# Kernel optimization log

Measured on AMD Instinct MI355X. Metric: run time of the kernel, lower is better.

The kernel has to match this reference:

```python
import jax, jax.numpy as jnp
import numpy as np
import math

D_MODEL = 1024
LAYER_ID = 6
NUM_LAYERS = 12
B = 8
T = 2048


def setup_inputs() -> dict:
    key = jax.random.key(0)
    ks = jax.random.split(key, 5)
    r01 = LAYER_ID / (NUM_LAYERS - 1)
    r1a0 = 1.0 - LAYER_ID / NUM_LAYERS
    h = np.arange(D_MODEL, dtype=np.float32)
    w = (-5.0 + 8.0 * (h / (D_MODEL - 1)) ** (0.7 + 1.3 * r01)).astype(np.float32)
    zigzag = np.array([(i + 1) % 3 - 1 for i in range(D_MODEL)], np.float32) * 0.5
    u = (np.ones(D_MODEL, np.float32) * math.log(0.3) + zigzag).astype(np.float32)
    xinit = (h / D_MODEL).astype(np.float32)
    tmk = (xinit ** r1a0).reshape(1, 1, D_MODEL).astype(np.float32)
    tmv = (tmk + 0.3 * r01).astype(np.float32)
    tmr = (xinit ** (0.5 * r1a0)).reshape(1, 1, D_MODEL).astype(np.float32)
    s = 1.0 / math.sqrt(D_MODEL)
    Wk = jax.random.normal(ks[0], (D_MODEL, D_MODEL), jnp.float32) * s
    Wv = jax.random.normal(ks[1], (D_MODEL, D_MODEL), jnp.float32) * s
    Wr = jax.random.normal(ks[2], (D_MODEL, D_MODEL), jnp.float32) * s
    Wo = jax.random.normal(ks[3], (D_MODEL, D_MODEL), jnp.float32) * s
    x = jax.random.normal(ks[4], (B, T, D_MODEL), jnp.float32)
    return dict(
        x=x,
        w=jnp.asarray(w), u=jnp.asarray(u),
        time_mix_k=jnp.asarray(tmk), time_mix_v=jnpp if False else jnp.asarray(tmv), time_mix_r=jnp.asarray(tmr),
        Wk=Wk, Wv=Wv, Wr=Wr, Wo=Wo,
    )


def _wkv(w, u, k, v):
    # w,u: [C] (raw params); k,v: [B,T,C]. Numerically-stable RWKV scan.
    wn = -jnp.exp(w)  # decay (negative)

    def step(carry, kv):
        aa, bb, pp = carry  # each [B,C]
        kt, vt = kv         # [B,C]
        ww = u + kt
        p = jnp.maximum(pp, ww)
        e1 = jnp.exp(pp - p)
        e2 = jnp.exp(ww - p)
        y = (e1 * aa + e2 * vt) / (e1 * bb + e2)
        ww2 = pp + wn
        p2 = jnp.maximum(ww2, kt)
        e1b = jnp.exp(ww2 - p2)
        e2b = jnp.exp(kt - p2)
        return (e1b * aa + e2b * vt, e1b * bb + e2b, p2), y

    Bd, Td, Cd = k.shape
    init = (jnp.zeros((Bd, Cd), k.dtype), jnp.zeros((Bd, Cd), k.dtype),
            jnp.full((Bd, Cd), -1e38, k.dtype))
    kT = jnp.swapaxes(k, 0, 1)  # [T,B,C]
    vT = jnp.swapaxes(v, 0, 1)
    _, ys = jax.lax.scan(step, init, (kT, vT))
    return jnp.swapaxes(ys, 0, 1)  # [B,T,C]


def reference(x, w, u, time_mix_k, time_mix_v, time_mix_r, Wk, Wv, Wr, Wo):
    # token shift: zero-pad one step at the front of time, drop last
    xs = jnp.pad(x, ((0, 0), (1, 0), (0, 0)))[:, :-1]
    xk = x * time_mix_k + xs * (1.0 - time_mix_k)
    xv = x * time_mix_v + xs * (1.0 - time_mix_v)
    xr = x * time_mix_r + xs * (1.0 - time_mix_r)
    k = jnp.einsum('btc,dc->btd', xk, Wk)
    v = jnp.einsum('btc,dc->btd', xv, Wv)
    r = jnp.einsum('btc,dc->btd', xr, Wr)
    wkv = _wkv(w, u, k, v)
    rwkv = jax.nn.sigmoid(r) * wkv
    return jnp.einsum('btc,dc->btd', rwkv, Wo)
```

## Files before the change

### kernel.cpp

```cpp
#include <hip/hip_runtime.h>
#include <hip/hip_bf16.h>
#include <stdint.h>

#define DM     1024
#define BATCH  8
#define SEQ    2048
#define MROWS  (BATCH * SEQ)
#define NCH    16
#define CHL    (SEQ / NCH)
#define CSTR   544

typedef unsigned short u16;
typedef __attribute__((ext_vector_type(8))) __bf16 bf16x8;
typedef __attribute__((ext_vector_type(4))) float  f32x4;

#define MB (1024ull * 1024ull)

__device__ __forceinline__ u16 f2bf(float f) {
    unsigned u = __float_as_uint(f);
    u += 0x7fffu + ((u >> 16) & 1u);
    return (u16)(u >> 16);
}
__device__ __forceinline__ float bf2f(u16 h) {
    return __uint_as_float(((unsigned)h) << 16);
}

__device__ __forceinline__ bool in_f32(const void* wraw) {
    return ((*(const unsigned*)wraw) & 0xFFFFu) == 0u;
}

__device__ __forceinline__ void ld16_lds(const u16* g, u16* l) {
    __builtin_amdgcn_global_load_lds(
        (const __attribute__((address_space(1))) void*)g,
        (__attribute__((address_space(3))) void*)l, 16, 0, 0);
}

__global__ __launch_bounds__(256) void mix_tile(
    const void* __restrict__ xraw,
    const void* __restrict__ tmkraw,
    const void* __restrict__ tmvraw,
    const void* __restrict__ tmrraw,
    const void* __restrict__ wraw,
    u16* __restrict__ xk, u16* __restrict__ xv, u16* __restrict__ xr)
{
    __shared__ u16 xt[18 * 1024];
    const bool f32i = in_f32(wraw);
    const int r0  = blockIdx.x * 16;
    const int t0  = r0 & (SEQ - 1);
    const int tid = threadIdx.x;
    const int c4  = tid * 4;

    float mk[4], mv[4], mr[4];
    if (f32i) {
        #pragma unroll
        for (int j = 0; j < 4; ++j) {
            mk[j] = ((const float*)tmkraw)[c4 + j];
            mv[j] = ((const float*)tmvraw)[c4 + j];
            mr[j] = ((const float*)tmrraw)[c4 + j];
        }
    } else {
        union { u16 h[4]; uint2 u; } a, b, c;
        a.u = *(const uint2*)((const u16*)tmkraw + c4);
        b.u = *(const uint2*)((const u16*)tmvraw + c4);
        c.u = *(const uint2*)((const u16*)tmrraw + c4);
        #pragma unroll
        for (int j = 0; j < 4; ++j) {
            mk[j] = bf2f(a.h[j]); mv[j] = bf2f(b.h[j]); mr[j] = bf2f(c.h[j]);
        }
    }

    #pragma unroll
    for (int p = 0; p < 9; ++p) {
        int lr = 2 * p + (tid >> 7);
        int gr = r0 - 1 + lr;
        if (lr == 0 && t0 == 0) gr = r0;
        if (gr >= MROWS) gr = r0;
        if (f32i) {
            const float* gp = (const float*)xraw + (size_t)gr * DM + (tid & 127) * 8;
            union { u16 h[8]; uint4 u; } t;
            #pragma unroll
            for (int j = 0; j < 8; ++j) t.h[j] = f2bf(gp[j]);
            *(uint4*)&xt[p * 2048 + tid * 8] = t.u;
        } else {
            const u16* gp = (const u16*)xraw + (size_t)gr * DM + (tid & 127) * 8;
            ld16_lds(gp, &xt[p * 2048 + (tid >> 6) * 512]);
        }
    }
    __syncthreads();

    const size_t obase = (size_t)r0 * DM + c4;
    #pragma unroll 4
    for (int rr = 0; rr < 16; ++rr) {
        union { u16 h[4]; uint2 u; } xa, xsv, ok, ov, orr;
        xa.u = *(const uint2*)&xt[(rr + 1) * 1024 + c4];
        float xf[4], sf[4];
        if (rr == 0 && t0 == 0) {
            #pragma unroll
            for (int j = 0; j < 4; ++j) sf[j] = 0.f;
        } else {
            xsv.u = *(const uint2*)&xt[rr * 1024 + c4];
            #pragma unroll
            for (int j = 0; j < 4; ++j) sf[j] = bf2f(xsv.h[j]);
        }
        #pragma unroll
        for (int j = 0; j < 4; ++j) xf[j] = bf2f(xa.h[j]);
        #pragma unroll
        for (int j = 0; j < 4; ++j) {
            float d = xf[j] - sf[j];
            ok.h[j]  = f2bf(sf[j] + mk[j] * d);
            ov.h[j]  = f2bf(sf[j] + mv[j] * d);
            orr.h[j] = f2bf(sf[j] + mr[j] * d);
        }
        size_t o = obase + (size_t)rr * DM;
        *(uint2*)(xk + o) = ok.u;
        *(uint2*)(xv + o) = ov.u;
        *(uint2*)(xr + o) = orr.u;
    }
}

__global__ void cast_w(const void* __restrict__ Wraw,
                       const void* __restrict__ wflag,
                       u16* __restrict__ Wb)
{
    int i = (blockIdx.x * 256 + threadIdx.x) << 2;
    if (in_f32(wflag)) {
        float4 wv = *(const float4*)((const float*)Wraw + i);
        union { u16 h[4]; uint2 u; } p;
        p.h[0] = f2bf(wv.x); p.h[1] = f2bf(wv.y);
        p.h[2] = f2bf(wv.z); p.h[3] = f2bf(wv.w);
        *(uint2*)(Wb + i) = p.u;
    } else {
        *(uint2*)(Wb + i) = *(const uint2*)((const u16*)Wraw + i);
    }
}

template <int NZ>
__global__ __launch_bounds__(256) void gemm_bt(
    const u16* __restrict__ A0, const u16* __restrict__ A1, const u16* __restrict__ A2,
    const u16* __restrict__ B0, const u16* __restrict__ B1, const u16* __restrict__ B2,
    void* __restrict__ C0, void* __restrict__ C1, void* __restrict__ C2,
    int c0f32)
{
    __shared__ u16 As[16 * CSTR];
    __shared__ u16 Bs[16 * CSTR];

    const int lin = blockIdx.x + (blockIdx.y << 3) + (blockIdx.z << 10);
    const int xcd = lin & 7;
    const int idx = lin >> 3;
    const int bxe = idx & 7;
    const int t   = idx >> 3;
    const int bye = xcd + ((t & 15) << 3);
    const int z   = t >> 4;

    const u16* A = (z == 0) ? A0 : (z == 1) ? A1 : A2;
    const u16* B = (z == 0) ? B0 : (z == 1) ? B1 : B2;
    void*      C = (z == 0) ? C0 : (z == 1) ? C1 : C2;
    const bool f32out = (z == 0) && c0f32;

    const int tid  = threadIdx.x;
    const int wave = tid >> 6, lane = tid & 63;
    const int wm   = wave >> 1, wn = wave & 1;
    const int lr   = lane & 15, quad = lane >> 4;
    const int tm   = bye * 128, tn = bxe * 128;
    const int srow  = lane >> 3;
    const int skoff = (lane & 7) * 8;

    f32x4 acc[4][4] = {};

    for (int k0 = 0; k0 < DM; k0 += 64) {
        #pragma unroll
        for (int i2 = 0; i2 < 4; ++i2) {
            int ch  = wave * 4 + i2;
            int row = ch * 8 + srow;
            ld16_lds(A + (size_t)(tm + row) * DM + k0 + skoff, &As[ch * CSTR]);
            ld16_lds(B + (size_t)(tn + row) * DM + k0 + skoff, &Bs[ch * CSTR]);
        }
        __syncthreads();
        #pragma unroll
        for (int kk2 = 0; kk2 < 2; ++kk2) {
            bf16x8 af[4], bfg[4];
            #pragma unroll
            for (int mi = 0; mi < 4; ++mi) {
                int r = wm * 64 + mi * 16 + lr;
                af[mi] = *(const bf16x8*)&As[(r >> 3) * CSTR + (r & 7) * 64 + kk2 * 32 + quad * 8];
            }
            #pragma unroll
            for (int ni = 0; ni < 4; ++ni) {
                int r = wn * 64 + ni * 16 + lr;
                bfg[ni] = *(const bf16x8*)&Bs[(r >> 3) * CSTR + (r & 7) * 64 + kk2 * 32 + quad * 8];
            }
            #pragma unroll
            for (int mi = 0; mi < 4; ++mi)
                #pragma unroll
                for (int ni = 0; ni < 4; ++ni)
                    acc[mi][ni] = __builtin_amdgcn_mfma_f32_16x16x32_bf16(
                        af[mi], bfg[ni], acc[mi][ni], 0, 0, 0);
        }
        __syncthreads();
    }
    #pragma unroll
    for (int mi = 0; mi < 4; ++mi)
        #pragma unroll
        for (int ni = 0; ni < 4; ++ni)
            #pragma unroll
            for (int r = 0; r < 4; ++r) {
                int row = tm + wm * 64 + mi * 16 + quad * 4 + r;
                int col = tn + wn * 64 + ni * 16 + lr;
                float v = acc[mi][ni][r];
                if (f32out) ((float*)C)[(size_t)row * DM + col] = v;
                else        ((u16*)C)[(size_t)row * DM + col]   = f2bf(v);
            }
}

__device__ __forceinline__ float ldval(const float* p) { return *p; }
__device__ __forceinline__ float ldval(const u16*  p) { return bf2f(*p); }

template <typename KT>
__global__ __launch_bounds__(256) void wkv_phase1(
    const KT* __restrict__ kk, const u16* __restrict__ vv,
    const void* __restrict__ wraw,
    float* __restrict__ sa, float* __restrict__ sb, float* __restrict__ sp)
{
    const int gid = blockIdx.x * 256 + threadIdx.x;
    const int c   = gid & (DM - 1);
    const int ch  = (gid >> 10) & (NCH - 1);
    const int b   = gid >> 14;
    float wc = in_f32(wraw) ? ((const float*)wraw)[c] : bf2f(((const u16*)wraw)[c]);
    const float wn = -__expf(wc);

    const size_t base = ((size_t)b * SEQ + (size_t)ch * CHL) * DM + c;
    float la = 0.f, lb = 0.f, lp = -1e38f;

    float kb[8], vb[8];
    #pragma unroll
    for (int j = 0; j < 8; ++j) {
        size_t id = base + (size_t)j * DM;
        kb[j] = ldval(kk + id); vb[j] = ldval(vv + id);
    }
    for (int t0 = 0; t0 < CHL; t0 += 8) {
        const bool more = (t0 + 8) < CHL;
        float kn[8], vn[8];
        if (more) {
            size_t nb = base + (size_t)(t0 + 8) * DM;
            #pragma unroll
            for (int j = 0; j < 8; ++j) {
                size_t id = nb + (size_t)j * DM;
                kn[j] = ldval(kk + id); vn[j] = ldval(vv + id);
            }
        }
        #pragma unroll
        for (int j = 0; j < 8; ++j) {
            const float kt = kb[j], vt = vb[j];
            const float w2 = lp + wn;
            const float p2 = fmaxf(w2, kt);
            const float e1 = __expf(w2 - p2);
            const float e2 = __expf(kt - p2);
            la = e1 * la + e2 * vt;
            lb = e1 * lb + e2;
            lp = p2;
        }
        if (more) {
            #pragma unroll
            for (int j = 0; j < 8; ++j) { kb[j] = kn[j]; vb[j] = vn[j]; }
        }
    }
    const int sidx = ((b * NCH + ch) << 10) + c;
    sa[sidx] = la; sb[sidx] = lb; sp[sidx] = lp;
}

__global__ __launch_bounds__(256) void wkv_combine(
    float* __restrict__ sa, float* __restrict__ sb, float* __restrict__ sp,
    const void* __restrict__ wraw)
{
    const int gid = blockIdx.x * 256 + threadIdx.x;
    const int c   = gid & (DM - 1);
    const int b   = gid >> 10;
    float wc = in_f32(wraw) ? ((const float*)wraw)[c] : bf2f(((const u16*)wraw)[c]);
    const float lamL = -__expf(wc) * (float)CHL;

    float aa = 0.f, bb = 0.f, pp = -1e38f;
    #pragma unroll
    for (int j = 0; j < NCH; ++j) {
        const int idx = ((b * NCH + j) << 10) + c;
        const float la = sa[idx], lb = sb[idx], lp = sp[idx];
        sa[idx] = aa; sb[idx] = bb; sp[idx] = pp;
        const float w2 = pp + lamL;
        const float np = fmaxf(w2, lp);
        const float e1 = __expf(w2 - np);
        const float e2 = __expf(lp - np);
        aa = e1 * aa + e2 * la;
        bb = e1 * bb + e2 * lb;
        pp = np;
    }
}

template <typename KT>
__global__ __launch_bounds__(256) void wkv_phase3(
    const KT* __restrict__ kk, const u16* __restrict__ vv,
    const u16* __restrict__ rr,
    const float* __restrict__ sa, const float* __restrict__ sb,
    const float* __restrict__ sp,
    const void* __restrict__ wraw, const void* __restrict__ uraw,
    u16* __restrict__ out)
{
    const int gid = blockIdx.x * 256 + threadIdx.x;
    const int c   = gid & (DM - 1);
    const int ch  = (gid >> 10) & (NCH - 1);
    const int b   = gid >> 14;
    float wc, uc;
    if (in_f32(wraw)) {
        wc = ((const float*)wraw)[c]; uc = ((const float*)uraw)[c];
    } else {
        wc = bf2f(((const u16*)wraw)[c]); uc = bf2f(((const u16*)uraw)[c]);
    }
    const float wn = -__expf(wc);
    const float uu = uc;

    const int sidx = ((b * NCH + ch) << 10) + c;
    float aa = sa[sidx], bb = sb[sidx], pp = sp[sidx];

    const size_t base = ((size_t)b * SEQ + (size_t)ch * CHL) * DM + c;

    float kb[8], vb[8], rb[8];
    #pragma unroll
    for (int j = 0; j < 8; ++j) {
        size_t id = base + (size_t)j * DM;
        kb[j] = ldval(kk + id); vb[j] = ldval(vv + id); rb[j] = ldval(rr + id);
    }
    for (int t0 = 0; t0 < CHL; t0 += 8) {
        const bool more = (t0 + 8) < CHL;
        float kn[8], vn[8], rn[8];
        if (more) {
            size_t nb = base + (size_t)(t0 + 8) * DM;
            #pragma unroll
            for (int j = 0; j < 8; ++j) {
                size_t id = nb + (size_t)j * DM;
                kn[j] = ldval(kk + id); vn[j] = ldval(vv + id); rn[j] = ldval(rr + id);
            }
        }
        #pragma unroll
        for (int j = 0; j < 8; ++j) {
            const float kt = kb[j], vt = vb[j], rt = rb[j];
            const float ww = uu + kt;
            const float p  = fmaxf(pp, ww);
            const float e1 = __expf(pp - p);
            const float e2 = __expf(ww - p);
            const float y  = (e1 * aa + e2 * vt) / (e1 * bb + e2);
            const float w2 = pp + wn;
            const float p2 = fmaxf(w2, kt);
            const float e1b = __expf(w2 - p2);
            const float e2b = __expf(kt - p2);
            aa = e1b * aa + e2b * vt;
            bb = e1b * bb + e2b;
            pp = p2;
            const float sr = 1.f / (1.f + __expf(-rt));
            out[base + (size_t)(t0 + j) * DM] = f2bf(sr * y);
        }
        if (more) {
            #pragma unroll
            for (int j = 0; j < 8; ++j) { kb[j] = kn[j]; vb[j] = vn[j]; rb[j] = rn[j]; }
        }
    }
}

extern "C" void kernel_launch(void* const* d_in, const int* in_sizes, int n_in,
                              void* d_out, int out_size, void* d_ws, size_t ws_size,
                              hipStream_t stream)
{
    const void* x   = d_in[0];
    const void* w   = d_in[1];
    const void* u   = d_in[2];
    const void* tmk = d_in[3];
    const void* tmv = d_in[4];
    const void* tmr = d_in[5];
    const void* Wk  = d_in[6];
    const void* Wv  = d_in[7];
    const void* Wr  = d_in[8];
    const void* Wo  = d_in[9];

    char* base = (char*)d_ws;
    const bool kf32 = ws_size >= 168 * MB;
    u16* Wkb  = (u16*)(base);
    u16* Wvb  = (u16*)(base + 2 * MB);
    u16* Wrb  = (u16*)(base + 4 * MB);
    u16* Wob  = (u16*)(base + 6 * MB);
    u16* xk   = (u16*)(base + 8 * MB);
    u16* xv   = (u16*)(base + 40 * MB);
    u16* xr   = (u16*)(base + 72 * MB);
    void* kbuf = (void*)(base + 104 * MB);
    u16* vb   = xk;
    u16* rb   = xv;
    u16* rwkv = xr;
    float* sa   = (float*)(base);
    float* sbuf = (float*)(base + 512 * 1024);
    float* sp   = (float*)(base + 1024 * 1024);

    cast_w<<<DM * DM / 1024, 256, 0, stream>>>(Wk, w, Wkb);
    cast_w<<<DM * DM / 1024, 256, 0, stream>>>(Wv, w, Wvb);
    cast_w<<<DM * DM / 1024, 256, 0, stream>>>(Wr, w, Wrb);
    cast_w<<<DM * DM / 1024, 256, 0, stream>>>(Wo, w, Wob);
    mix_tile<<<MROWS / 16, 256, 0, stream>>>(x, tmk, tmv, tmr, w, xk, xv, xr);

    gemm_bt<3><<<dim3(8, 128, 3), 256, 0, stream>>>(
        xk, xv, xr, Wkb, Wvb, Wrb, kbuf, vb, rb, kf32 ? 1 : 0);

    const int scan_threads = BATCH * NCH * DM;
    if (kf32) {
        wkv_phase1<float><<<scan_threads / 256, 256, 0, stream>>>(
            (const float*)kbuf, vb, w, sa, sbuf, sp);
        wkv_combine<<<BATCH * DM / 256, 256, 0, stream>>>(sa, sbuf, sp, w);
        wkv_phase3<float><<<scan_threads / 256, 256, 0, stream>>>(
            (const float*)kbuf, vb, rb, sa, sbuf, sp, w, u, rwkv);
    } else {
        wkv_phase1<u16><<<scan_threads / 256, 256, 0, stream>>>(
            (const u16*)kbuf, vb, w, sa, sbuf, sp);
        wkv_combine<<<BATCH * DM / 256, 256, 0, stream>>>(sa, sbuf, sp, w);
        wkv_phase3<u16><<<scan_threads / 256, 256, 0, stream>>>(
            (const u16*)kbuf, vb, rb, sa, sbuf, sp, w, u, rwkv);
    }

    gemm_bt<1><<<dim3(8, 128, 1), 256, 0, stream>>>(
        rwkv, rwkv, rwkv, Wob, Wob, Wob, d_out, d_out, d_out, 1);
}
```

Measured before the change: 413.9 us.

## Rewrite bf16 GEMM with 256x256 tiles, double-buffered LDS and XOR swizzle

The GEMM kernel moves from 128x128 tiles with 4 waves to 256x256 tiles with 8 waves, so each block reuses more operand data per load. LDS is now double-buffered, with the next tile's A and B loads issued between MFMA groups under explicit waitcnt and barrier control. An XOR swizzle replaces the padded LDS stride to avoid bank conflicts. This uses 128KB of LDS per block and more accumulator registers, which lowers occupancy, and the grid shrinks to 768 and 256 blocks, which risks poorer load balance across CUs.

```diff
diff --git a/kernel.cpp b/kernel.cpp
--- a/kernel.cpp
+++ b/kernel.cpp
@@ -8,7 +8,7 @@
 #define MROWS  (BATCH * SEQ)
 #define NCH    16
 #define CHL    (SEQ / NCH)
-#define CSTR   544
+#define NT     (DM / 64)
 
 typedef unsigned short u16;
 typedef __attribute__((ext_vector_type(8))) __bf16 bf16x8;
@@ -135,78 +135,127 @@
 }
 
 template <int NZ>
-__global__ __launch_bounds__(256) void gemm_bt(
+__global__ __launch_bounds__(512) void gemm_bt(
     const u16* __restrict__ A0, const u16* __restrict__ A1, const u16* __restrict__ A2,
     const u16* __restrict__ B0, const u16* __restrict__ B1, const u16* __restrict__ B2,
     void* __restrict__ C0, void* __restrict__ C1, void* __restrict__ C2,
     int c0f32)
 {
-    __shared__ u16 As[16 * CSTR];
-    __shared__ u16 Bs[16 * CSTR];
-
-    const int lin = blockIdx.x + (blockIdx.y << 3) + (blockIdx.z << 10);
+    __shared__ u16 As[2][256 * 64];
+    __shared__ u16 Bs[2][256 * 64];
+
+    const int lin = blockIdx.x;
     const int xcd = lin & 7;
     const int idx = lin >> 3;
-    const int bxe = idx & 7;
-    const int t   = idx >> 3;
-    const int bye = xcd + ((t & 15) << 3);
-    const int z   = t >> 4;
-
-    const u16* A = (z == 0) ? A0 : (z == 1) ? A1 : A2;
-    const u16* B = (z == 0) ? B0 : (z == 1) ? B1 : B2;
+    const int z   = idx >> 5;
+    const int r   = idx & 31;
+    const int bxe = r & 3;
+    const int bye = xcd + ((r >> 2) << 3);
+
+    const u16* __restrict__ A = (z == 0) ? A0 : (z == 1) ? A1 : A2;
+    const u16* __restrict__ B = (z == 0) ? B0 : (z == 1) ? B1 : B2;
     void*      C = (z == 0) ? C0 : (z == 1) ? C1 : C2;
     const bool f32out = (z == 0) && c0f32;
 
     const int tid  = threadIdx.x;
-    const int wave = tid >> 6, lane = tid & 63;
-    const int wm   = wave >> 1, wn = wave & 1;
+    const int w    = tid >> 6, lane = tid & 63;
+    const int wm   = w >> 2, wn = w & 3;
     const int lr   = lane & 15, quad = lane >> 4;
-    const int tm   = bye * 128, tn = bxe * 128;
-    const int srow  = lane >> 3;
-    const int skoff = (lane & 7) * 8;
-
-    f32x4 acc[4][4] = {};
-
-    for (int k0 = 0; k0 < DM; k0 += 64) {
-        #pragma unroll
-        for (int i2 = 0; i2 < 4; ++i2) {
-            int ch  = wave * 4 + i2;
-            int row = ch * 8 + srow;
-            ld16_lds(A + (size_t)(tm + row) * DM + k0 + skoff, &As[ch * CSTR]);
-            ld16_lds(B + (size_t)(tn + row) * DM + k0 + skoff, &Bs[ch * CSTR]);
-        }
-        __syncthreads();
-        #pragma unroll
-        for (int kk2 = 0; kk2 < 2; ++kk2) {
-            bf16x8 af[4], bfg[4];
-            #pragma unroll
-            for (int mi = 0; mi < 4; ++mi) {
-                int r = wm * 64 + mi * 16 + lr;
-                af[mi] = *(const bf16x8*)&As[(r >> 3) * CSTR + (r & 7) * 64 + kk2 * 32 + quad * 8];
-            }
-            #pragma unroll
-            for (int ni = 0; ni < 4; ++ni) {
-                int r = wn * 64 + ni * 16 + lr;
-                bfg[ni] = *(const bf16x8*)&Bs[(r >> 3) * CSTR + (r & 7) * 64 + kk2 * 32 + quad * 8];
-            }
-            #pragma unroll
-            for (int mi = 0; mi < 4; ++mi)
-                #pragma unroll
-                for (int ni = 0; ni < 4; ++ni)
-                    acc[mi][ni] = __builtin_amdgcn_mfma_f32_16x16x32_bf16(
-                        af[mi], bfg[ni], acc[mi][ni], 0, 0, 0);
-        }
-        __syncthreads();
-    }
-    #pragma unroll
-    for (int mi = 0; mi < 4; ++mi)
+    const int tm   = bye * 256, tn = bxe * 256;
+
+    const int srow = lane >> 3;
+    const int scol = ((lane & 7) ^ srow) * 8;
+    const u16* srcA = A + (size_t)(tm + srow) * DM + scol;
+    const u16* srcB = B + (size_t)(tn + srow) * DM + scol;
+
+    const int sw0 = (quad * 8) ^ ((lr & 7) * 8);
+    const int sw1 = (32 + quad * 8) ^ ((lr & 7) * 8);
+    const int arowb = (wm * 128 + lr) * 64;
+    const int browb = (wn * 64 + lr) * 64;
+
+    f32x4 acc[8][4] = {};
+
+    auto stageA = [&](int t, int j) {
+        int row = j * 64 + w * 8;
+        ld16_lds(srcA + (size_t)row * DM + t * 64, &As[t & 1][row * 64]);
+    };
+    auto stageB = [&](int t, int j) {
+        int row = j * 64 + w * 8;
+        ld16_lds(srcB + (size_t)row * DM + t * 64, &Bs[t & 1][row * 64]);
+    };
+
+    #pragma unroll
+    for (int j = 0; j < 4; ++j) stageA(0, j);
+    #pragma unroll
+    for (int j = 0; j < 4; ++j) stageB(0, j);
+    #pragma unroll
+    for (int j = 0; j < 4; ++j) stageA(1, j);
+    asm volatile("s_waitcnt vmcnt(4)" ::: "memory");
+    __builtin_amdgcn_s_barrier();
+
+    bf16x8 af[8], bfr[4];
+
+#define MFMA_PAIR(NI0)                                                        \
+    __builtin_amdgcn_s_barrier();                                             \
+    asm volatile("s_waitcnt lgkmcnt(0)" ::: "memory");                        \
+    __builtin_amdgcn_s_setprio(1);                                            \
+    _Pragma("unroll")                                                         \
+    for (int mi = 0; mi < 8; ++mi) {                                          \
+        acc[mi][NI0]     = __builtin_amdgcn_mfma_f32_16x16x32_bf16(           \
+            af[mi], bfr[NI0],     acc[mi][NI0],     0, 0, 0);                 \
+        acc[mi][NI0 + 1] = __builtin_amdgcn_mfma_f32_16x16x32_bf16(           \
+            af[mi], bfr[NI0 + 1], acc[mi][NI0 + 1], 0, 0, 0);                 \
+    }                                                                         \
+    __builtin_amdgcn_s_setprio(0);                                            \
+    __builtin_amdgcn_s_barrier();
+
+    #pragma unroll 2
+    for (int t = 0; t < NT; ++t) {
+        const u16* __restrict__ Ab = As[t & 1];
+        const u16* __restrict__ Bb = Bs[t & 1];
+
+        #pragma unroll
+        for (int mi = 0; mi < 8; ++mi)
+            af[mi] = *(const bf16x8*)&Ab[arowb + mi * 1024 + sw0];
+        bfr[0] = *(const bf16x8*)&Bb[browb + sw0];
+        bfr[1] = *(const bf16x8*)&Bb[browb + 1024 + sw0];
+        if (t + 1 < NT) { stageB(t + 1, 0); stageB(t + 1, 1); }
+        MFMA_PAIR(0)
+
+        bfr[2] = *(const bf16x8*)&Bb[browb + 2048 + sw0];
+        bfr[3] = *(const bf16x8*)&Bb[browb + 3072 + sw0];
+        if (t + 1 < NT) { stageB(t + 1, 2); stageB(t + 1, 3); }
+        MFMA_PAIR(2)
+
+        #pragma unroll
+        for (int mi = 0; mi < 8; ++mi)
+            af[mi] = *(const bf16x8*)&Ab[arowb + mi * 1024 + sw1];
+        bfr[0] = *(const bf16x8*)&Bb[browb + sw1];
+        bfr[1] = *(const bf16x8*)&Bb[browb + 1024 + sw1];
+        MFMA_PAIR(0)
+
+        bfr[2] = *(const bf16x8*)&Bb[browb + 2048 + sw1];
+        bfr[3] = *(const bf16x8*)&Bb[browb + 3072 + sw1];
+        if (t + 2 < NT) {
+            #pragma unroll
+            for (int j = 0; j < 4; ++j) stageA(t + 2, j);
+            asm volatile("s_waitcnt vmcnt(4)" ::: "memory");
+        } else {
+            asm volatile("s_waitcnt vmcnt(0)" ::: "memory");
+        }
+        MFMA_PAIR(2)
+    }
+#undef MFMA_PAIR
+
+    #pragma unroll
+    for (int mi = 0; mi < 8; ++mi)
         #pragma unroll
         for (int ni = 0; ni < 4; ++ni)
             #pragma unroll
-            for (int r = 0; r < 4; ++r) {
-                int row = tm + wm * 64 + mi * 16 + quad * 4 + r;
+            for (int rr = 0; rr < 4; ++rr) {
+                int row = tm + wm * 128 + mi * 16 + quad * 4 + rr;
                 int col = tn + wn * 64 + ni * 16 + lr;
-                float v = acc[mi][ni][r];
+                float v = acc[mi][ni][rr];
                 if (f32out) ((float*)C)[(size_t)row * DM + col] = v;
                 else        ((u16*)C)[(size_t)row * DM + col]   = f2bf(v);
             }
@@ -401,7 +450,7 @@
     cast_w<<<DM * DM / 1024, 256, 0, stream>>>(Wo, w, Wob);
     mix_tile<<<MROWS / 16, 256, 0, stream>>>(x, tmk, tmv, tmr, w, xk, xv, xr);
 
-    gemm_bt<3><<<dim3(8, 128, 3), 256, 0, stream>>>(
+    gemm_bt<3><<<768, 512, 0, stream>>>(
         xk, xv, xr, Wkb, Wvb, Wrb, kbuf, vb, rb, kf32 ? 1 : 0);
 
     const int scan_threads = BATCH * NCH * DM;
@@ -419,6 +468,6 @@
             (const u16*)kbuf, vb, rb, sa, sbuf, sp, w, u, rwkv);
     }
 
-    gemm_bt<1><<<dim3(8, 128, 1), 256, 0, stream>>>(
+    gemm_bt<1><<<256, 512, 0, stream>>>(
         rwkv, rwkv, rwkv, Wob, Wob, Wob, d_out, d_out, d_out, 1);
 }
```

Result: faster. 380.7 us (-8.0%).
